# Kernel optimization log

Hardware: AMD Instinct MI355X
Metric: run time of the kernel (lower is better)

The kernel has to match this reference:

```python
import jax, jax.numpy as jnp
import numpy as np

IN_C, HID, L, NN, BS, OUT = 32, 128, 4, 64, 512, 3
N = NN * BS  # total graph vertices
EPS_LN = 1e-5
EPS_SM = 1e-16  # PyG softmax eps


def setup_inputs() -> dict:
    key = jax.random.key(0)
    ks = jax.random.split(key, 16)
    E = 524288
    x = jax.random.normal(ks[0], (N, IN_C), dtype=jnp.float32)
    edge_index = jax.random.randint(ks[1], (2, E), 0, N, dtype=jnp.int64)
    s = 0.1
    # first GAT layer (in -> hidden)
    W0 = jax.random.normal(ks[2], (IN_C, HID), dtype=jnp.float32) * s
    att_src0 = jax.random.normal(ks[3], (HID,), dtype=jnp.float32) * s
    att_dst0 = jax.random.normal(ks[4], (HID,), dtype=jnp.float32) * s
    bias0 = jnp.zeros((HID,), dtype=jnp.float32)
    # residual GAT layers (hidden -> hidden), stacked over L
    W_res = jax.random.normal(ks[5], (L, HID, HID), dtype=jnp.float32) * s
    att_src_res = jax.random.normal(ks[6], (L, HID), dtype=jnp.float32) * s
    att_dst_res = jax.random.normal(ks[7], (L, HID), dtype=jnp.float32) * s
    bias_res = jnp.zeros((L, HID), dtype=jnp.float32)
    gamma = jnp.ones((L, HID), dtype=jnp.float32)
    beta = jnp.zeros((L, HID), dtype=jnp.float32)
    # per-node predictor heads
    W1p = jax.random.normal(ks[8], (NN, HID, HID // 2), dtype=jnp.float32) * s
    W2p = jax.random.normal(ks[9], (NN, HID // 2, OUT), dtype=jnp.float32) * s
    return {"x": x, "edge_index": edge_index, "W0": W0, "att_src0": att_src0,
            "att_dst0": att_dst0, "bias0": bias0, "W_res": W_res,
            "att_src_res": att_src_res, "att_dst_res": att_dst_res,
            "bias_res": bias_res, "gamma": gamma, "beta": beta,
            "W1p": W1p, "W2p": W2p}


def _gat(x, src, dst, W, a_src, a_dst, b):
    # PyG GATConv, heads=1, negative_slope=0.2, self-loops already appended
    h = x @ W                                   # [N, H]
    a_s = (h * a_src).sum(-1)                   # [N]
    a_d = (h * a_dst).sum(-1)                   # [N]
    e = jax.nn.leaky_relu(a_s[src] + a_d[dst], 0.2)   # [E]
    m = jax.ops.segment_max(e, dst, num_segments=N)
    e = jnp.exp(e - m[dst])
    z = jax.ops.segment_sum(e, dst, num_segments=N)
    alpha = e / (z[dst] + EPS_SM)               # [E]
    out = jax.ops.segment_sum(h[src] * alpha[:, None], dst, num_segments=N)
    return out + b


def _layernorm(x, g, b):
    mu = x.mean(-1, keepdims=True)
    var = ((x - mu) ** 2).mean(-1, keepdims=True)
    return (x - mu) * jax.lax.rsqrt(var + EPS_LN) * g + b


def reference(x, edge_index, W0, att_src0, att_dst0, bias0, W_res,
              att_src_res, att_dst_res, bias_res, gamma, beta, W1p, W2p):
    loops = jnp.arange(N, dtype=edge_index.dtype)
    src = jnp.concatenate([edge_index[0], loops])
    dst = jnp.concatenate([edge_index[1], loops])
    # first GAT + relu
    h = jax.nn.relu(_gat(x, src, dst, W0, att_src0, att_dst0, bias0))
    # res+ blocks: h = h + conv(dropout(act(norm(h))))  (dropout=identity, eval)
    for i in range(L):
        t = jax.nn.relu(_layernorm(h, gamma[i], beta[i]))
        t = _gat(t, src, dst, W_res[i], att_src_res[i], att_dst_res[i], bias_res[i])
        h = h + t
    h = jax.nn.relu(_layernorm(h, gamma[0], beta[0]))
    # per-node predictor heads
    h = h.reshape(NN, BS, HID)
    t = jax.nn.relu(jnp.einsum('nbh,nhk->nbk', h, W1p))
    logits = jnp.einsum('nbk,nko->nbo', t, W2p)
    return jax.nn.softmax(logits, axis=-1)   # softmax over class dim (dim=1 per node slice)
```

## Files before the change

### kernel.cpp

```cpp
#include <hip/hip_runtime.h>
#include <hip/hip_fp8.h>
#include <math.h>

#define NND   32768
#define HIDD  128
#define NHEAD 64
#define BSS   512
#define OUTC  3
#define NTILES (NND / 16)
#define CSLOT 80

typedef _Float16 half_t;
typedef __attribute__((ext_vector_type(8))) _Float16 half8;
typedef __attribute__((ext_vector_type(4))) float f32x4;

__device__ __forceinline__ unsigned enc_fp8x4(float a, float b, float c, float d) {
    __hip_fp8x4_e4m3 q(make_float4(a, b, c, d));
    return (unsigned)q.__x;
}
__device__ __forceinline__ float4 dec_fp8x4(unsigned v) {
    __hip_fp8x4_e4m3 t; t.__x = (__hip_fp8x4_storage_t)v;
    return (float4)t;
}

__global__ __launch_bounds__(256) void prep_kernel(const float* __restrict__ W0,
        const float* __restrict__ W_res, const float* __restrict__ W1p,
        const float* __restrict__ as0, const float* __restrict__ ad0,
        const float* __restrict__ as_res, const float* __restrict__ ad_res,
        const float* __restrict__ x, const int* __restrict__ ei, int E,
        half_t* __restrict__ Wh, half_t* __restrict__ W1h, half_t* __restrict__ W0t,
        float* __restrict__ wvec, half_t* __restrict__ xh,
        int* __restrict__ counts, int* __restrict__ csrd) {
    int b = blockIdx.x, tid = threadIdx.x;
    if (b < 64) {
        __shared__ float tile[32][33];
        int l = b >> 4, t = b & 15;
        int k0 = (t >> 2) * 32, n0 = (t & 3) * 32;
        const float* src = W_res + (size_t)l * 128 * 128;
        half_t* dst = Wh + (size_t)l * 128 * 128;
        int c = tid & 31, r0 = tid >> 5;
#pragma unroll
        for (int i = 0; i < 4; ++i) tile[r0 + i * 8][c] = src[(size_t)(k0 + r0 + i * 8) * 128 + n0 + c];
        __syncthreads();
#pragma unroll
        for (int i = 0; i < 4; ++i) dst[(size_t)(n0 + r0 + i * 8) * 128 + k0 + c] = (half_t)tile[c][r0 + i * 8];
    } else if (b < 576) {
        __shared__ float tile[32][33];
        int bb = b - 64, head = bb >> 3, t = bb & 7;
        int k0 = (t >> 1) * 32, n0 = (t & 1) * 32;
        const float* src = W1p + (size_t)head * 128 * 64;
        half_t* dst = W1h + (size_t)head * 64 * 128;
        int c = tid & 31, r0 = tid >> 5;
#pragma unroll
        for (int i = 0; i < 4; ++i) tile[r0 + i * 8][c] = src[(size_t)(k0 + r0 + i * 8) * 64 + n0 + c];
        __syncthreads();
#pragma unroll
        for (int i = 0; i < 4; ++i) dst[(size_t)(n0 + r0 + i * 8) * 128 + k0 + c] = (half_t)tile[c][r0 + i * 8];
    } else if (b == 576) {
        __shared__ float t0[32][129];
        for (int i = tid; i < 4096; i += 256) t0[i >> 7][i & 127] = W0[i];
        __syncthreads();
        for (int i = tid; i < 4096; i += 256) { int n = i >> 5, k = i & 31; W0t[n * 32 + k] = (half_t)t0[k][n]; }
    } else if (b == 577) {
        for (int task = tid; task < 1088; task += 256) {
            const float* row; const float* att; int slot, sd;
            if (task < 64) {
                int k = task >> 1; sd = task & 1;
                row = W0 + k * 128; att = sd ? ad0 : as0; slot = k;
            } else {
                int tt = task - 64; int l = 1 + tt / 256; int r = tt % 256;
                int k = r >> 1; sd = r & 1;
                row = W_res + (size_t)(l - 1) * 16384 + k * 128;
                att = (sd ? ad_res : as_res) + (l - 1) * 128;
                slot = l * 128 + k;
            }
            float s = 0.f;
            for (int n = 0; n < 128; ++n) s += row[n] * att[n];
            (sd ? wvec + 640 : wvec)[slot] = s;
        }
    } else if (b < 1090) {
        int b2 = b - 578;
        const float* xs = x + (size_t)b2 * 64 * 32;
        half_t* xd = xh + (size_t)b2 * 64 * 32;
        for (int i = tid; i < 1024; i += 256) {
            float2 v = ((const float2*)xs)[i];
            union { unsigned u; half_t h[2]; } cv;
            cv.h[0] = (half_t)v.x; cv.h[1] = (half_t)v.y;
            ((unsigned*)xd)[i] = cv.u;
        }
    } else {
        int j = (b - 1090) * 256 + tid;
        int Etot = E + NND;
        if (j >= Etot) return;
        int src, dst;
        if (j < E) { src = ei[j]; dst = ei[E + j]; }
        else       { src = j - E; dst = j - E; }
        int rank = atomicAdd(&counts[dst], 1);
        if (rank < CSLOT) csrd[(size_t)dst * CSLOT + rank] = src;
    }
}

__global__ __launch_bounds__(256) void a0_kernel(const half_t* __restrict__ xh,
        const float* __restrict__ wvec,
        float* __restrict__ a_s, float* __restrict__ a_d) {
    int tid = threadIdx.x;
    __shared__ float ws0[32], wd0[32];
    if (tid < 32) { ws0[tid] = wvec[tid]; wd0[tid] = wvec[640 + tid]; }
    __syncthreads();
    int g = blockIdx.x * 256 + tid;
    int node = g >> 2, part = g & 3;
    half8 xv = *(const half8*)&xh[(size_t)node * 32 + part * 8];
    float s = 0.f, d2 = 0.f;
#pragma unroll
    for (int j = 0; j < 8; ++j) { float f = (float)xv[j]; s += f * ws0[part * 8 + j]; d2 += f * wd0[part * 8 + j]; }
    s += __shfl_xor(s, 1); s += __shfl_xor(s, 2);
    d2 += __shfl_xor(d2, 1); d2 += __shfl_xor(d2, 2);
    if (part == 0) { a_s[node] = s; a_d[node] = d2; }
}


struct MArgs {
    const half_t* xh;
    const int* csrd;
    const int* counts;
    const half_t* W0t;
    const half_t* Wh;
    const float* bias0;
    const float* b_res;
    const float* gamma;
    const float* beta;
    const float* wvec;
    float* a_s0; float* a_d0; float* a_s1; float* a_d1;
    unsigned char* Th8a; unsigned char* Th8b;
    half_t* Hh;
    const half_t* W1h;
    const float* W2p;
    float* out;
};

struct SmemT {
    half_t Pt[16][136];
    union U {
        float vv[16][132];
        struct { int s[1024]; float p[1024]; } sp;
    } u;
    int cntl[16];
    float adv[16];
};

__device__ __forceinline__ void stage_sp(const float* __restrict__ a_sv,
        const int* __restrict__ csrd, int n0, int base, int tid, SmemT& sm) {
#pragma unroll
    for (int it = 0; it < 4; ++it) {
        int i = it * 256 + tid;
        int ln = i >> 6, k = i & 63;
        int sN = 0; float pN = 0.f;
        if (base + k < sm.cntl[ln]) {
            sN = csrd[(size_t)(n0 + ln) * CSLOT + base + k];
            float tt = a_sv[sN] + sm.adv[ln];
            tt = (tt > 0.f) ? tt : 0.2f * tt;
            pN = __expf(tt);
        }
        sm.u.sp.s[i] = sN;
        sm.u.sp.p[i] = pN;
    }
}

__device__ __forceinline__ void agg2_res(const unsigned char* __restrict__ F8,
        const float* __restrict__ a_sv, const float* __restrict__ a_dv,
        const int* __restrict__ csrd, const int* __restrict__ counts,
        int n0, int tid, int wv, int lane, int q, int r15, SmemT& sm) {
    if (tid < 16) { sm.cntl[tid] = counts[n0 + tid]; sm.adv[tid] = a_dv[n0 + tid]; }
    __syncthreads();
    int maxd = 0;
    for (int i = 0; i < 16; ++i) { int d = sm.cntl[i]; maxd = d > maxd ? d : maxd; }
    float acc[4][8];
    float pz[4];
#pragma unroll
    for (int a = 0; a < 4; ++a) {
        pz[a] = 0.f;
#pragma unroll
        for (int i = 0; i < 8; ++i) acc[a][i] = 0.f;
    }
    for (int base = 0; base < maxd; base += 64) {
        __syncthreads();
        stage_sp(a_sv, csrd, n0, base, tid, sm);
        __syncthreads();
#pragma unroll
        for (int ln4 = 0; ln4 < 4; ++ln4) {
            int ln = wv * 4 + ln4;
            int rem = sm.cntl[ln] - base;
            if (rem <= 0) continue;
            int cnt = rem > 64 ? 64 : rem;
            pz[ln4] += sm.u.sp.p[ln * 64 + lane];
            const int* sl = &sm.u.sp.s[ln * 64];
            const float* pl = &sm.u.sp.p[ln * 64];
            for (int k4 = 0; k4 < cnt; k4 += 16) {
                int s0 = sl[k4 + q],      s1 = sl[k4 + 4 + q];
                int s2 = sl[k4 + 8 + q],  s3 = sl[k4 + 12 + q];
                float p0 = pl[k4 + q],    p1 = pl[k4 + 4 + q];
                float p2 = pl[k4 + 8 + q], p3 = pl[k4 + 12 + q];
                uint2 r0 = *(const uint2*)&F8[(size_t)s0 * HIDD + r15 * 8];
                uint2 r1 = *(const uint2*)&F8[(size_t)s1 * HIDD + r15 * 8];
                uint2 r2 = *(const uint2*)&F8[(size_t)s2 * HIDD + r15 * 8];
                uint2 r3 = *(const uint2*)&F8[(size_t)s3 * HIDD + r15 * 8];
                float4 f;
                f = dec_fp8x4(r0.x); acc[ln4][0]+=p0*f.x; acc[ln4][1]+=p0*f.y; acc[ln4][2]+=p0*f.z; acc[ln4][3]+=p0*f.w;
                f = dec_fp8x4(r0.y); acc[ln4][4]+=p0*f.x; acc[ln4][5]+=p0*f.y; acc[ln4][6]+=p0*f.z; acc[ln4][7]+=p0*f.w;
                f = dec_fp8x4(r1.x); acc[ln4][0]+=p1*f.x; acc[ln4][1]+=p1*f.y; acc[ln4][2]+=p1*f.z; acc[ln4][3]+=p1*f.w;
                f = dec_fp8x4(r1.y); acc[ln4][4]+=p1*f.x; acc[ln4][5]+=p1*f.y; acc[ln4][6]+=p1*f.z; acc[ln4][7]+=p1*f.w;
                f = dec_fp8x4(r2.x); acc[ln4][0]+=p2*f.x; acc[ln4][1]+=p2*f.y; acc[ln4][2]+=p2*f.z; acc[ln4][3]+=p2*f.w;
                f = dec_fp8x4(r2.y); acc[ln4][4]+=p2*f.x; acc[ln4][5]+=p2*f.y; acc[ln4][6]+=p2*f.z; acc[ln4][7]+=p2*f.w;
                f = dec_fp8x4(r3.x); acc[ln4][0]+=p3*f.x; acc[ln4][1]+=p3*f.y; acc[ln4][2]+=p3*f.z; acc[ln4][3]+=p3*f.w;
                f = dec_fp8x4(r3.y); acc[ln4][4]+=p3*f.x; acc[ln4][5]+=p3*f.y; acc[ln4][6]+=p3*f.z; acc[ln4][7]+=p3*f.w;
            }
        }
    }
#pragma unroll
    for (int ln4 = 0; ln4 < 4; ++ln4) {
        int ln = wv * 4 + ln4;
        float z = pz[ln4];
#pragma unroll
        for (int o = 32; o; o >>= 1) z += __shfl_xor(z, o);
#pragma unroll
        for (int i = 0; i < 8; ++i) {
            acc[ln4][i] += __shfl_xor(acc[ln4][i], 16);
            acc[ln4][i] += __shfl_xor(acc[ln4][i], 32);
        }
        if (q == 0) {
            float inv = 1.f / (z + 1e-16f);
            union { int4 v; half_t hh[8]; } u;
#pragma unroll
            for (int i = 0; i < 8; ++i) u.hh[i] = (half_t)(acc[ln4][i] * inv);
            *(int4*)&sm.Pt[ln][r15 * 8] = u.v;
        }
    }
}

__device__ __forceinline__ void agg2_l0(const half_t* __restrict__ xh,
        const float* __restrict__ a_sv, const float* __restrict__ a_dv,
        const int* __restrict__ csrd, const int* __restrict__ counts,
        int n0, int tid, int wv, int lane, int q, int r15, SmemT& sm) {
    if (tid < 16) { sm.cntl[tid] = counts[n0 + tid]; sm.adv[tid] = a_dv[n0 + tid]; }
    __syncthreads();
    int maxd = 0;
    for (int i = 0; i < 16; ++i) { int d = sm.cntl[i]; maxd = d > maxd ? d : maxd; }
    float acc[4][2];
    float pz[4];
#pragma unroll
    for (int a = 0; a < 4; ++a) { pz[a] = 0.f; acc[a][0] = 0.f; acc[a][1] = 0.f; }
    for (int base = 0; base < maxd; base += 64) {
        __syncthreads();
        stage_sp(a_sv, csrd, n0, base, tid, sm);
        __syncthreads();
#pragma unroll
        for (int ln4 = 0; ln4 < 4; ++ln4) {
            int ln = wv * 4 + ln4;
            int rem = sm.cntl[ln] - base;
            if (rem <= 0) continue;
            int cnt = rem > 64 ? 64 : rem;
            pz[ln4] += sm.u.sp.p[ln * 64 + lane];
            const int* sl = &sm.u.sp.s[ln * 64];
            const float* pl = &sm.u.sp.p[ln * 64];
            for (int k4 = 0; k4 < cnt; k4 += 16) {
                int s0 = sl[k4 + q],      s1 = sl[k4 + 4 + q];
                int s2 = sl[k4 + 8 + q],  s3 = sl[k4 + 12 + q];
                float p0 = pl[k4 + q],    p1 = pl[k4 + 4 + q];
                float p2 = pl[k4 + 8 + q], p3 = pl[k4 + 12 + q];
                union { unsigned u; half_t h[2]; } u0, u1, u2, u3;
                u0.u = *(const unsigned*)&xh[(size_t)s0 * 32 + r15 * 2];
                u1.u = *(const unsigned*)&xh[(size_t)s1 * 32 + r15 * 2];
                u2.u = *(const unsigned*)&xh[(size_t)s2 * 32 + r15 * 2];
                u3.u = *(const unsigned*)&xh[(size_t)s3 * 32 + r15 * 2];
                acc[ln4][0] += p0 * (float)u0.h[0] + p1 * (float)u1.h[0] + p2 * (float)u2.h[0] + p3 * (float)u3.h[0];
                acc[ln4][1] += p0 * (float)u0.h[1] + p1 * (float)u1.h[1] + p2 * (float)u2.h[1] + p3 * (float)u3.h[1];
            }
        }
    }
#pragma unroll
    for (int ln4 = 0; ln4 < 4; ++ln4) {
        int ln = wv * 4 + ln4;
        float z = pz[ln4];
#pragma unroll
        for (int o = 32; o; o >>= 1) z += __shfl_xor(z, o);
#pragma unroll
        for (int i = 0; i < 2; ++i) {
            acc[ln4][i] += __shfl_xor(acc[ln4][i], 16);
            acc[ln4][i] += __shfl_xor(acc[ln4][i], 32);
        }
        if (q == 0) {
            float inv = 1.f / (z + 1e-16f);
            union { unsigned u; half_t h[2]; } w2;
            w2.h[0] = (half_t)(acc[ln4][0] * inv);
            w2.h[1] = (half_t)(acc[ln4][1] * inv);
            *(unsigned*)&sm.Pt[ln][r15 * 2] = w2.u;
        }
    }
}

template <int K, bool RES>
__device__ __forceinline__ void gemm_epi_tile(int n0, int tid, int wv, int q, int r15,
        const half_t* __restrict__ Whl, const float* __restrict__ bias,
        half_t* __restrict__ Hh, unsigned char* __restrict__ Th8o,
        const float* __restrict__ gamma, const float* __restrict__ beta,
        const float* __restrict__ wsn, const float* __restrict__ wdn,
        float* __restrict__ as_out, float* __restrict__ ad_out,
        half_t Pt[16][136], float vv[16][132]) {
    half8 afrag[K / 32];
#pragma unroll
    for (int s = 0; s < K / 32; ++s)
        afrag[s] = *(const half8*)&Pt[r15][s * 32 + q * 8];
    f32x4 acc2[2];
#pragma unroll
    for (int i = 0; i < 2; ++i) {
        int ct = wv * 2 + i;
        f32x4 c = {0.f, 0.f, 0.f, 0.f};
#pragma unroll
        for (int s = 0; s < K / 32; ++s) {
            half8 bfrag = *(const half8*)&Whl[(size_t)(ct * 16 + r15) * K + s * 32 + q * 8];
            c = __builtin_amdgcn_mfma_f32_16x16x32_f16(afrag[s], bfrag, c, 0, 0, 0);
        }
        acc2[i] = c;
    }
#pragma unroll
    for (int i = 0; i < 2; ++i)
#pragma unroll
        for (int r = 0; r < 4; ++r)
            vv[q * 4 + r][wv * 32 + i * 16 + r15] = acc2[i][r];
    __syncthreads();
    int grp = tid >> 4, sub = tid & 15;
    float4 bi0 = *(const float4*)&bias[sub * 8],  bi1 = *(const float4*)&bias[sub * 8 + 4];
    float4 g0  = *(const float4*)&gamma[sub * 8], g1  = *(const float4*)&gamma[sub * 8 + 4];
    float4 be0 = *(const float4*)&beta[sub * 8],  be1 = *(const float4*)&beta[sub * 8 + 4];
    float4 ws0 = *(const float4*)&wsn[sub * 8],   ws1 = *(const float4*)&wsn[sub * 8 + 4];
    float4 wd0 = *(const float4*)&wdn[sub * 8],   wd1 = *(const float4*)&wdn[sub * 8 + 4];
    float bi[8] = {bi0.x,bi0.y,bi0.z,bi0.w,bi1.x,bi1.y,bi1.z,bi1.w};
    float gg[8] = {g0.x,g0.y,g0.z,g0.w,g1.x,g1.y,g1.z,g1.w};
    float be[8] = {be0.x,be0.y,be0.z,be0.w,be1.x,be1.y,be1.z,be1.w};
    float ws[8] = {ws0.x,ws0.y,ws0.z,ws0.w,ws1.x,ws1.y,ws1.z,ws1.w};
    float wd[8] = {wd0.x,wd0.y,wd0.z,wd0.w,wd1.x,wd1.y,wd1.z,wd1.w};
    int node = n0 + grp;
    float v8[8];
#pragma unroll
    for (int j = 0; j < 8; ++j) v8[j] = vv[grp][sub * 8 + j] + bi[j];
    if (RES) {
        half8 hold = *(const half8*)&Hh[(size_t)node * HIDD + sub * 8];
#pragma unroll
        for (int j = 0; j < 8; ++j) v8[j] += (float)hold[j];
    } else {
#pragma unroll
        for (int j = 0; j < 8; ++j) v8[j] = fmaxf(v8[j], 0.f);
    }
    union { int4 i4; half_t h[8]; } hw;
#pragma unroll
    for (int j = 0; j < 8; ++j) hw.h[j] = (half_t)v8[j];
    *(int4*)&Hh[(size_t)node * HIDD + sub * 8] = hw.i4;
    float sum = 0.f;
#pragma unroll
    for (int j = 0; j < 8; ++j) sum += v8[j];
#pragma unroll
    for (int o = 8; o; o >>= 1) sum += __shfl_xor(sum, o);
    float mu = sum * (1.f / HIDD);
    float var = 0.f;
#pragma unroll
    for (int j = 0; j < 8; ++j) { float dx = v8[j] - mu; var += dx * dx; }
#pragma unroll
    for (int o = 8; o; o >>= 1) var += __shfl_xor(var, o);
    float rs = rsqrtf(var * (1.f / HIDD) + 1e-5f);
    float tt[8];
    float asn = 0.f, adn = 0.f;
#pragma unroll
    for (int j = 0; j < 8; ++j) {
        float t = fmaxf((v8[j] - mu) * rs * gg[j] + be[j], 0.f);
        tt[j] = t;
        asn += t * ws[j];
        adn += t * wd[j];
    }
    uint2 tw;
    tw.x = enc_fp8x4(tt[0], tt[1], tt[2], tt[3]);
    tw.y = enc_fp8x4(tt[4], tt[5], tt[6], tt[7]);
    *(uint2*)&Th8o[(size_t)node * HIDD + sub * 8] = tw;
#pragma unroll
    for (int o = 8; o; o >>= 1) { asn += __shfl_xor(asn, o); adn += __shfl_xor(adn, o); }
    if (sub == 0) { as_out[node] = asn; ad_out[node] = adn; }
}

__device__ __forceinline__ void last_tile(int n0, int tid, int wv, int q, int r15,
        const MArgs& A, half_t Pt[16][136], float vv[16][132]) {
    const half_t* Whl = A.Wh + (size_t)3 * 16384;
    half8 afrag[4];
#pragma unroll
    for (int s = 0; s < 4; ++s)
        afrag[s] = *(const half8*)&Pt[r15][s * 32 + q * 8];
    f32x4 acc2[2];
#pragma unroll
    for (int i = 0; i < 2; ++i) {
        int ct = wv * 2 + i;
        f32x4 c = {0.f, 0.f, 0.f, 0.f};
#pragma unroll
        for (int s = 0; s < 4; ++s) {
            half8 bfrag = *(const half8*)&Whl[(size_t)(ct * 16 + r15) * 128 + s * 32 + q * 8];
            c = __builtin_amdgcn_mfma_f32_16x16x32_f16(afrag[s], bfrag, c, 0, 0, 0);
        }
        acc2[i] = c;
    }
#pragma unroll
    for (int i = 0; i < 2; ++i)
#pragma unroll
        for (int r = 0; r < 4; ++r)
            vv[q * 4 + r][wv * 32 + i * 16 + r15] = acc2[i][r];
    __syncthreads();
    int grp = tid >> 4, sub = tid & 15;
    const float* bias = A.b_res + 3 * HIDD;
    float4 bi0 = *(const float4*)&bias[sub * 8],    bi1 = *(const float4*)&bias[sub * 8 + 4];
    float4 g0  = *(const float4*)&A.gamma[sub * 8], g1  = *(const float4*)&A.gamma[sub * 8 + 4];
    float4 be0 = *(const float4*)&A.beta[sub * 8],  be1 = *(const float4*)&A.beta[sub * 8 + 4];
    float bi[8] = {bi0.x,bi0.y,bi0.z,bi0.w,bi1.x,bi1.y,bi1.z,bi1.w};
    float gg[8] = {g0.x,g0.y,g0.z,g0.w,g1.x,g1.y,g1.z,g1.w};
    float be[8] = {be0.x,be0.y,be0.z,be0.w,be1.x,be1.y,be1.z,be1.w};
    int node = n0 + grp;
    float v8[8];
    half8 hold = *(const half8*)&A.Hh[(size_t)node * HIDD + sub * 8];
#pragma unroll
    for (int j = 0; j < 8; ++j) v8[j] = vv[grp][sub * 8 + j] + bi[j] + (float)hold[j];
    float sum = 0.f;
#pragma unroll
    for (int j = 0; j < 8; ++j) sum += v8[j];
#pragma unroll
    for (int o = 8; o; o >>= 1) sum += __shfl_xor(sum, o);
    float mu = sum * (1.f / HIDD);
    float var = 0.f;
#pragma unroll
    for (int j = 0; j < 8; ++j) { float dx = v8[j] - mu; var += dx * dx; }
#pragma unroll
    for (int o = 8; o; o >>= 1) var += __shfl_xor(var, o);
    float rs = rsqrtf(var * (1.f / HIDD) + 1e-5f);
    union { int4 i4; half_t h[8]; } u;
#pragma unroll
    for (int j = 0; j < 8; ++j)
        u.h[j] = (half_t)fmaxf((v8[j] - mu) * rs * gg[j] + be[j], 0.f);
    __syncthreads();
    *(int4*)&Pt[grp][sub * 8] = u.i4;
    __syncthreads();
    int head = n0 >> 9;
    const half_t* W1g = A.W1h + (size_t)head * 64 * 128;
    half8 pa[4];
#pragma unroll
    for (int s = 0; s < 4; ++s)
        pa[s] = *(const half8*)&Pt[r15][s * 32 + q * 8];
    int n2 = wv * 16 + r15;
    f32x4 c = {0.f, 0.f, 0.f, 0.f};
#pragma unroll
    for (int s = 0; s < 4; ++s) {
        half8 bfrag = *(const half8*)&W1g[(size_t)n2 * 128 + s * 32 + q * 8];
        c = __builtin_amdgcn_mfma_f32_16x16x32_f16(pa[s], bfrag, c, 0, 0, 0);
    }
    float w2a = A.W2p[(size_t)head * 192 + n2 * 3 + 0];
    float w2b = A.W2p[(size_t)head * 192 + n2 * 3 + 1];
    float w2c = A.W2p[(size_t)head * 192 + n2 * 3 + 2];
    float lg[3][4];
#pragma unroll
    for (int r = 0; r < 4; ++r) {
        float t = fmaxf(c[r], 0.f);
        lg[0][r] = t * w2a;
        lg[1][r] = t * w2b;
        lg[2][r] = t * w2c;
    }
#pragma unroll
    for (int o = 8; o; o >>= 1)
#pragma unroll
        for (int oo = 0; oo < 3; ++oo)
#pragma unroll
            for (int r = 0; r < 4; ++r) lg[oo][r] += __shfl_xor(lg[oo][r], o);
    __syncthreads();
    if (r15 == 0) {
#pragma unroll
        for (int r = 0; r < 4; ++r)
#pragma unroll
            for (int oo = 0; oo < 3; ++oo) vv[q * 4 + r][wv * 3 + oo] = lg[oo][r];
    }
    __syncthreads();
    if (tid < 16) {
        float l0 = vv[tid][0] + vv[tid][3] + vv[tid][6] + vv[tid][9];
        float l1 = vv[tid][1] + vv[tid][4] + vv[tid][7] + vv[tid][10];
        float l2 = vv[tid][2] + vv[tid][5] + vv[tid][8] + vv[tid][11];
        float mx = fmaxf(l0, fmaxf(l1, l2));
        float e0 = __expf(l0 - mx), e1 = __expf(l1 - mx), e2 = __expf(l2 - mx);
        float inv = 1.f / (e0 + e1 + e2);
        float* op = A.out + (size_t)(n0 + tid) * OUTC;
        op[0] = e0 * inv; op[1] = e1 * inv; op[2] = e2 * inv;
    }
}

__global__ __launch_bounds__(256, 4) void fused3_l0(MArgs A) {
    __shared__ SmemT sm;
    int tid = threadIdx.x;
    int wv = tid >> 6, lane = tid & 63;
    int q = lane >> 4, r15 = lane & 15;
    int n0 = blockIdx.x * 16;
    agg2_l0(A.xh, A.a_s0, A.a_d0, A.csrd, A.counts, n0, tid, wv, lane, q, r15, sm);
    __syncthreads();
    gemm_epi_tile<32, false>(n0, tid, wv, q, r15, A.W0t, A.bias0, A.Hh, A.Th8a,
        A.gamma, A.beta, A.wvec + 128, A.wvec + 640 + 128, A.a_s1, A.a_d1, sm.Pt, sm.u.vv);
}

template <int L>
__global__ __launch_bounds__(256, 4) void fused3_res(MArgs A) {
    __shared__ SmemT sm;
    int tid = threadIdx.x;
    int wv = tid >> 6, lane = tid & 63;
    int q = lane >> 4, r15 = lane & 15;
    int n0 = blockIdx.x * 16;
    const unsigned char* Ts = (L & 1) ? A.Th8b : A.Th8a;
    unsigned char* Td       = (L & 1) ? A.Th8a : A.Th8b;
    const float* asv = (L & 1) ? A.a_s0 : A.a_s1;
    const float* adv = (L & 1) ? A.a_d0 : A.a_d1;
    float* aso = (L & 1) ? A.a_s1 : A.a_s0;
    float* ado = (L & 1) ? A.a_d1 : A.a_d0;
    agg2_res(Ts, asv, adv, A.csrd, A.counts, n0, tid, wv, lane, q, r15, sm);
    __syncthreads();
    gemm_epi_tile<128, true>(n0, tid, wv, q, r15, A.Wh + (size_t)L * 16384,
        A.b_res + L * HIDD, A.Hh, Td, A.gamma + (L + 1) * HIDD, A.beta + (L + 1) * HIDD,
        A.wvec + (L + 2) * 128, A.wvec + 640 + (L + 2) * 128, aso, ado, sm.Pt, sm.u.vv);
}

__global__ __launch_bounds__(256, 4) void fused3_last(MArgs A) {
    __shared__ SmemT sm;
    int tid = threadIdx.x;
    int wv = tid >> 6, lane = tid & 63;
    int q = lane >> 4, r15 = lane & 15;
    int n0 = blockIdx.x * 16;
    agg2_res(A.Th8b, A.a_s0, A.a_d0, A.csrd, A.counts, n0, tid, wv, lane, q, r15, sm);
    __syncthreads();
    last_tile(n0, tid, wv, q, r15, A, sm.Pt, sm.u.vv);
}

extern "C" void kernel_launch(void* const* d_in, const int* in_sizes, int n_in,
                              void* d_out, int out_size, void* d_ws, size_t ws_size,
                              hipStream_t stream) {
    const float* x        = (const float*)d_in[0];
    const int*   ei       = (const int*)d_in[1];
    const float* W0       = (const float*)d_in[2];
    const float* att_src0 = (const float*)d_in[3];
    const float* att_dst0 = (const float*)d_in[4];
    const float* bias0    = (const float*)d_in[5];
    const float* W_res    = (const float*)d_in[6];
    const float* as_res   = (const float*)d_in[7];
    const float* ad_res   = (const float*)d_in[8];
    const float* b_res    = (const float*)d_in[9];
    const float* gamma    = (const float*)d_in[10];
    const float* beta     = (const float*)d_in[11];
    const float* W1p      = (const float*)d_in[12];
    const float* W2p      = (const float*)d_in[13];
    float* out = (float*)d_out;

    int E = in_sizes[1] / 2;
    int Etot = E + NND;

    char* p = (char*)d_ws;
    auto alloc = [&](size_t bytes) { void* r = (void*)p; p += (bytes + 255) & ~(size_t)255; return r; };
    int*    counts  = (int*)alloc((size_t)NND * 4);
    int*    csrd    = (int*)alloc((size_t)NND * CSLOT * 4);
    half_t* xh      = (half_t*)alloc((size_t)NND * 32 * 2);
    unsigned char* Th8a = (unsigned char*)alloc((size_t)NND * HIDD);
    unsigned char* Th8b = (unsigned char*)alloc((size_t)NND * HIDD);
    half_t* Hh      = (half_t*)alloc((size_t)NND * HIDD * 2);
    float*  a_s0    = (float*)alloc((size_t)NND * 4);
    float*  a_d0    = (float*)alloc((size_t)NND * 4);
    float*  a_s1    = (float*)alloc((size_t)NND * 4);
    float*  a_d1    = (float*)alloc((size_t)NND * 4);
    half_t* Wh      = (half_t*)alloc((size_t)4 * HIDD * HIDD * 2);
    half_t* W1h     = (half_t*)alloc((size_t)NHEAD * 64 * HIDD * 2);
    half_t* W0t     = (half_t*)alloc((size_t)HIDD * 32 * 2);
    float*  wvec    = (float*)alloc((size_t)1280 * 4);

    int egrid = (Etot + 255) / 256;

    hipMemsetAsync(counts, 0, (size_t)NND * 4, stream);
    prep_kernel<<<1090 + egrid, 256, 0, stream>>>(W0, W_res, W1p, att_src0, att_dst0,
        as_res, ad_res, x, ei, E, Wh, W1h, W0t, wvec, xh, counts, csrd);
    a0_kernel<<<512, 256, 0, stream>>>(xh, wvec, a_s0, a_d0);

    MArgs ma;
    ma.xh = xh; ma.csrd = csrd; ma.counts = counts;
    ma.W0t = W0t; ma.Wh = Wh;
    ma.bias0 = bias0; ma.b_res = b_res;
    ma.gamma = gamma; ma.beta = beta; ma.wvec = wvec;
    ma.a_s0 = a_s0; ma.a_d0 = a_d0; ma.a_s1 = a_s1; ma.a_d1 = a_d1;
    ma.Th8a = Th8a; ma.Th8b = Th8b; ma.Hh = Hh;
    ma.W1h = W1h; ma.W2p = W2p; ma.out = out;

    fused3_l0<<<NTILES, 256, 0, stream>>>(ma);
    fused3_res<0><<<NTILES, 256, 0, stream>>>(ma);
    fused3_res<1><<<NTILES, 256, 0, stream>>>(ma);
    fused3_res<2><<<NTILES, 256, 0, stream>>>(ma);
    fused3_last<<<NTILES, 256, 0, stream>>>(ma);
}
```

Measured before the change: 277.6 us.

## Cut register pressure in GAT aggregation and epilogue to raise occupancy

Splits the residual aggregation into two passes of two nodes each, so only 2x8 accumulators are live instead of 4x8. Adds a fast path that stages neighbor data once when every node in the tile has at most 64 edges. Reorders the epilogue to load gamma, beta and the attention vectors in smaller chunks, and raises launch bounds to 8 waves per SIMD for the l0 and residual kernels. The goal is higher occupancy to hide gather latency. In exchange, the multi-chunk path now restages the CSR slice once per pass, and the tighter register cap risks spills.

```diff
diff --git a/kernel.cpp b/kernel.cpp
--- a/kernel.cpp
+++ b/kernel.cpp
@@ -31,9 +31,9 @@
         half_t* __restrict__ Wh, half_t* __restrict__ W1h, half_t* __restrict__ W0t,
         float* __restrict__ wvec, half_t* __restrict__ xh,
         int* __restrict__ counts, int* __restrict__ csrd) {
+    __shared__ float tile[32][129];
     int b = blockIdx.x, tid = threadIdx.x;
     if (b < 64) {
-        __shared__ float tile[32][33];
         int l = b >> 4, t = b & 15;
         int k0 = (t >> 2) * 32, n0 = (t & 3) * 32;
         const float* src = W_res + (size_t)l * 128 * 128;
@@ -45,7 +45,6 @@
 #pragma unroll
         for (int i = 0; i < 4; ++i) dst[(size_t)(n0 + r0 + i * 8) * 128 + k0 + c] = (half_t)tile[c][r0 + i * 8];
     } else if (b < 576) {
-        __shared__ float tile[32][33];
         int bb = b - 64, head = bb >> 3, t = bb & 7;
         int k0 = (t >> 1) * 32, n0 = (t & 1) * 32;
         const float* src = W1p + (size_t)head * 128 * 64;
@@ -57,10 +56,9 @@
 #pragma unroll
         for (int i = 0; i < 4; ++i) dst[(size_t)(n0 + r0 + i * 8) * 128 + k0 + c] = (half_t)tile[c][r0 + i * 8];
     } else if (b == 576) {
-        __shared__ float t0[32][129];
-        for (int i = tid; i < 4096; i += 256) t0[i >> 7][i & 127] = W0[i];
+        for (int i = tid; i < 4096; i += 256) tile[i >> 7][i & 127] = W0[i];
         __syncthreads();
-        for (int i = tid; i < 4096; i += 256) { int n = i >> 5, k = i & 31; W0t[n * 32 + k] = (half_t)t0[k][n]; }
+        for (int i = tid; i < 4096; i += 256) { int n = i >> 5, k = i & 31; W0t[n * 32 + k] = (half_t)tile[k][n]; }
     } else if (b == 577) {
         for (int task = tid; task < 1088; task += 256) {
             const float* row; const float* att; int slot, sd;
@@ -166,6 +164,59 @@
     }
 }
 
+__device__ __forceinline__ void agg_node_f8(const unsigned char* __restrict__ F8,
+        const SmemT& sm, int ln, int base, int lane, int q, int r15,
+        float acc[8], float& pzv) {
+    int rem = sm.cntl[ln] - base;
+    if (rem <= 0) return;
+    int cnt = rem > 64 ? 64 : rem;
+    pzv += sm.u.sp.p[ln * 64 + lane];
+    const int* sl = &sm.u.sp.s[ln * 64];
+    const float* pl = &sm.u.sp.p[ln * 64];
+    for (int k4 = 0; k4 < cnt; k4 += 16) {
+        int s0 = sl[k4 + q],       s1 = sl[k4 + 4 + q];
+        int s2 = sl[k4 + 8 + q],   s3 = sl[k4 + 12 + q];
+        float p0 = pl[k4 + q],     p1 = pl[k4 + 4 + q];
+        float p2 = pl[k4 + 8 + q], p3 = pl[k4 + 12 + q];
+        uint2 r0 = *(const uint2*)&F8[(size_t)s0 * HIDD + r15 * 8];
+        uint2 r1 = *(const uint2*)&F8[(size_t)s1 * HIDD + r15 * 8];
+        uint2 r2 = *(const uint2*)&F8[(size_t)s2 * HIDD + r15 * 8];
+        uint2 r3 = *(const uint2*)&F8[(size_t)s3 * HIDD + r15 * 8];
+        float4 f;
+        f = dec_fp8x4(r0.x); acc[0]+=p0*f.x; acc[1]+=p0*f.y; acc[2]+=p0*f.z; acc[3]+=p0*f.w;
+        f = dec_fp8x4(r0.y); acc[4]+=p0*f.x; acc[5]+=p0*f.y; acc[6]+=p0*f.z; acc[7]+=p0*f.w;
+        f = dec_fp8x4(r1.x); acc[0]+=p1*f.x; acc[1]+=p1*f.y; acc[2]+=p1*f.z; acc[3]+=p1*f.w;
+        f = dec_fp8x4(r1.y); acc[4]+=p1*f.x; acc[5]+=p1*f.y; acc[6]+=p1*f.z; acc[7]+=p1*f.w;
+        f = dec_fp8x4(r2.x); acc[0]+=p2*f.x; acc[1]+=p2*f.y; acc[2]+=p2*f.z; acc[3]+=p2*f.w;
+        f = dec_fp8x4(r2.y); acc[4]+=p2*f.x; acc[5]+=p2*f.y; acc[6]+=p2*f.z; acc[7]+=p2*f.w;
+        f = dec_fp8x4(r3.x); acc[0]+=p3*f.x; acc[1]+=p3*f.y; acc[2]+=p3*f.z; acc[3]+=p3*f.w;
+        f = dec_fp8x4(r3.y); acc[4]+=p3*f.x; acc[5]+=p3*f.y; acc[6]+=p3*f.z; acc[7]+=p3*f.w;
+    }
+}
+
+__device__ __forceinline__ void finish_res(SmemT& sm, int wv, int pass, int q, int r15,
+        float acc[2][8], float pz2[2]) {
+#pragma unroll
+    for (int ln2 = 0; ln2 < 2; ++ln2) {
+        int ln = wv * 4 + pass * 2 + ln2;
+        float z = pz2[ln2];
+#pragma unroll
+        for (int o = 32; o; o >>= 1) z += __shfl_xor(z, o);
+#pragma unroll
+        for (int i = 0; i < 8; ++i) {
+            acc[ln2][i] += __shfl_xor(acc[ln2][i], 16);
+            acc[ln2][i] += __shfl_xor(acc[ln2][i], 32);
+        }
+        if (q == 0) {
+            float inv = 1.f / (z + 1e-16f);
+            union { int4 v; half_t hh[8]; } u;
+#pragma unroll
+            for (int i = 0; i < 8; ++i) u.hh[i] = (half_t)(acc[ln2][i] * inv);
+            *(int4*)&sm.Pt[ln][r15 * 8] = u.v;
+        }
+    }
+}
+
 __device__ __forceinline__ void agg2_res(const unsigned char* __restrict__ F8,
         const float* __restrict__ a_sv, const float* __restrict__ a_dv,
         const int* __restrict__ csrd, const int* __restrict__ counts,
@@ -174,65 +225,40 @@
     __syncthreads();
     int maxd = 0;
     for (int i = 0; i < 16; ++i) { int d = sm.cntl[i]; maxd = d > maxd ? d : maxd; }
-    float acc[4][8];
-    float pz[4];
-#pragma unroll
-    for (int a = 0; a < 4; ++a) {
-        pz[a] = 0.f;
-#pragma unroll
-        for (int i = 0; i < 8; ++i) acc[a][i] = 0.f;
-    }
-    for (int base = 0; base < maxd; base += 64) {
+    if (maxd <= 64) {
+        stage_sp(a_sv, csrd, n0, 0, tid, sm);
         __syncthreads();
-        stage_sp(a_sv, csrd, n0, base, tid, sm);
-        __syncthreads();
-#pragma unroll
-        for (int ln4 = 0; ln4 < 4; ++ln4) {
-            int ln = wv * 4 + ln4;
-            int rem = sm.cntl[ln] - base;
-            if (rem <= 0) continue;
-            int cnt = rem > 64 ? 64 : rem;
-            pz[ln4] += sm.u.sp.p[ln * 64 + lane];
-            const int* sl = &sm.u.sp.s[ln * 64];
-            const float* pl = &sm.u.sp.p[ln * 64];
-            for (int k4 = 0; k4 < cnt; k4 += 16) {
-                int s0 = sl[k4 + q],      s1 = sl[k4 + 4 + q];
-                int s2 = sl[k4 + 8 + q],  s3 = sl[k4 + 12 + q];
-                float p0 = pl[k4 + q],    p1 = pl[k4 + 4 + q];
-                float p2 = pl[k4 + 8 + q], p3 = pl[k4 + 12 + q];
-                uint2 r0 = *(const uint2*)&F8[(size_t)s0 * HIDD + r15 * 8];
-                uint2 r1 = *(const uint2*)&F8[(size_t)s1 * HIDD + r15 * 8];
-                uint2 r2 = *(const uint2*)&F8[(size_t)s2 * HIDD + r15 * 8];
-                uint2 r3 = *(const uint2*)&F8[(size_t)s3 * HIDD + r15 * 8];
-                float4 f;
-                f = dec_fp8x4(r0.x); acc[ln4][0]+=p0*f.x; acc[ln4][1]+=p0*f.y; acc[ln4][2]+=p0*f.z; acc[ln4][3]+=p0*f.w;
-                f = dec_fp8x4(r0.y); acc[ln4][4]+=p0*f.x; acc[ln4][5]+=p0*f.y; acc[ln4][6]+=p0*f.z; acc[ln4][7]+=p0*f.w;
-                f = dec_fp8x4(r1.x); acc[ln4][0]+=p1*f.x; acc[ln4][1]+=p1*f.y; acc[ln4][2]+=p1*f.z; acc[ln4][3]+=p1*f.w;
-                f = dec_fp8x4(r1.y); acc[ln4][4]+=p1*f.x; acc[ln4][5]+=p1*f.y; acc[ln4][6]+=p1*f.z; acc[ln4][7]+=p1*f.w;
-                f = dec_fp8x4(r2.x); acc[ln4][0]+=p2*f.x; acc[ln4][1]+=p2*f.y; acc[ln4][2]+=p2*f.z; acc[ln4][3]+=p2*f.w;
-                f = dec_fp8x4(r2.y); acc[ln4][4]+=p2*f.x; acc[ln4][5]+=p2*f.y; acc[ln4][6]+=p2*f.z; acc[ln4][7]+=p2*f.w;
-                f = dec_fp8x4(r3.x); acc[ln4][0]+=p3*f.x; acc[ln4][1]+=p3*f.y; acc[ln4][2]+=p3*f.z; acc[ln4][3]+=p3*f.w;
-                f = dec_fp8x4(r3.y); acc[ln4][4]+=p3*f.x; acc[ln4][5]+=p3*f.y; acc[ln4][6]+=p3*f.z; acc[ln4][7]+=p3*f.w;
+#pragma unroll
+        for (int pass = 0; pass < 2; ++pass) {
+            float acc[2][8];
+            float pz2[2] = {0.f, 0.f};
+#pragma unroll
+            for (int a = 0; a < 2; ++a)
+#pragma unroll
+                for (int i = 0; i < 8; ++i) acc[a][i] = 0.f;
+#pragma unroll
+            for (int ln2 = 0; ln2 < 2; ++ln2)
+                agg_node_f8(F8, sm, wv * 4 + pass * 2 + ln2, 0, lane, q, r15, acc[ln2], pz2[ln2]);
+            finish_res(sm, wv, pass, q, r15, acc, pz2);
+        }
+    } else {
+#pragma unroll
+        for (int pass = 0; pass < 2; ++pass) {
+            float acc[2][8];
+            float pz2[2] = {0.f, 0.f};
+#pragma unroll
+            for (int a = 0; a < 2; ++a)
+#pragma unroll
+                for (int i = 0; i < 8; ++i) acc[a][i] = 0.f;
+            for (int base = 0; base < maxd; base += 64) {
+                __syncthreads();
+                stage_sp(a_sv, csrd, n0, base, tid, sm);
+                __syncthreads();
+#pragma unroll
+                for (int ln2 = 0; ln2 < 2; ++ln2)
+                    agg_node_f8(F8, sm, wv * 4 + pass * 2 + ln2, base, lane, q, r15, acc[ln2], pz2[ln2]);
             }
-        }
-    }
-#pragma unroll
-    for (int ln4 = 0; ln4 < 4; ++ln4) {
-        int ln = wv * 4 + ln4;
-        float z = pz[ln4];
-#pragma unroll
-        for (int o = 32; o; o >>= 1) z += __shfl_xor(z, o);
-#pragma unroll
-        for (int i = 0; i < 8; ++i) {
-            acc[ln4][i] += __shfl_xor(acc[ln4][i], 16);
-            acc[ln4][i] += __shfl_xor(acc[ln4][i], 32);
-        }
-        if (q == 0) {
-            float inv = 1.f / (z + 1e-16f);
-            union { int4 v; half_t hh[8]; } u;
-#pragma unroll
-            for (int i = 0; i < 8; ++i) u.hh[i] = (half_t)(acc[ln4][i] * inv);
-            *(int4*)&sm.Pt[ln][r15 * 8] = u.v;
+            finish_res(sm, wv, pass, q, r15, acc, pz2);
         }
     }
 }
@@ -329,20 +355,17 @@
             vv[q * 4 + r][wv * 32 + i * 16 + r15] = acc2[i][r];
     __syncthreads();
     int grp = tid >> 4, sub = tid & 15;
-    float4 bi0 = *(const float4*)&bias[sub * 8],  bi1 = *(const float4*)&bias[sub * 8 + 4];
-    float4 g0  = *(const float4*)&gamma[sub * 8], g1  = *(const float4*)&gamma[sub * 8 + 4];
-    float4 be0 = *(const float4*)&beta[sub * 8],  be1 = *(const float4*)&beta[sub * 8 + 4];
-    float4 ws0 = *(const float4*)&wsn[sub * 8],   ws1 = *(const float4*)&wsn[sub * 8 + 4];
-    float4 wd0 = *(const float4*)&wdn[sub * 8],   wd1 = *(const float4*)&wdn[sub * 8 + 4];
-    float bi[8] = {bi0.x,bi0.y,bi0.z,bi0.w,bi1.x,bi1.y,bi1.z,bi1.w};
-    float gg[8] = {g0.x,g0.y,g0.z,g0.w,g1.x,g1.y,g1.z,g1.w};
-    float be[8] = {be0.x,be0.y,be0.z,be0.w,be1.x,be1.y,be1.z,be1.w};
-    float ws[8] = {ws0.x,ws0.y,ws0.z,ws0.w,ws1.x,ws1.y,ws1.z,ws1.w};
-    float wd[8] = {wd0.x,wd0.y,wd0.z,wd0.w,wd1.x,wd1.y,wd1.z,wd1.w};
     int node = n0 + grp;
+    const float* vrow = &vv[grp][sub * 8];
     float v8[8];
-#pragma unroll
-    for (int j = 0; j < 8; ++j) v8[j] = vv[grp][sub * 8 + j] + bi[j];
+    {
+        float4 bi0 = *(const float4*)&bias[sub * 8];
+        float4 bi1 = *(const float4*)&bias[sub * 8 + 4];
+        v8[0] = vrow[0] + bi0.x; v8[1] = vrow[1] + bi0.y;
+        v8[2] = vrow[2] + bi0.z; v8[3] = vrow[3] + bi0.w;
+        v8[4] = vrow[4] + bi1.x; v8[5] = vrow[5] + bi1.y;
+        v8[6] = vrow[6] + bi1.z; v8[7] = vrow[7] + bi1.w;
+    }
     if (RES) {
         half8 hold = *(const half8*)&Hh[(size_t)node * HIDD + sub * 8];
 #pragma unroll
@@ -367,18 +390,34 @@
 #pragma unroll
     for (int o = 8; o; o >>= 1) var += __shfl_xor(var, o);
     float rs = rsqrtf(var * (1.f / HIDD) + 1e-5f);
-    float tt[8];
-    float asn = 0.f, adn = 0.f;
-#pragma unroll
-    for (int j = 0; j < 8; ++j) {
-        float t = fmaxf((v8[j] - mu) * rs * gg[j] + be[j], 0.f);
-        tt[j] = t;
-        asn += t * ws[j];
-        adn += t * wd[j];
-    }
+    float asn, adn;
     uint2 tw;
-    tw.x = enc_fp8x4(tt[0], tt[1], tt[2], tt[3]);
-    tw.y = enc_fp8x4(tt[4], tt[5], tt[6], tt[7]);
+    {
+        float4 g4 = *(const float4*)&gamma[sub * 8];
+        float4 b4 = *(const float4*)&beta[sub * 8];
+        float t0 = fmaxf((v8[0] - mu) * rs * g4.x + b4.x, 0.f);
+        float t1 = fmaxf((v8[1] - mu) * rs * g4.y + b4.y, 0.f);
+        float t2 = fmaxf((v8[2] - mu) * rs * g4.z + b4.z, 0.f);
+        float t3 = fmaxf((v8[3] - mu) * rs * g4.w + b4.w, 0.f);
+        float4 w4 = *(const float4*)&wsn[sub * 8];
+        float4 d4 = *(const float4*)&wdn[sub * 8];
+        asn = t0 * w4.x; asn += t1 * w4.y; asn += t2 * w4.z; asn += t3 * w4.w;
+        adn = t0 * d4.x; adn += t1 * d4.y; adn += t2 * d4.z; adn += t3 * d4.w;
+        tw.x = enc_fp8x4(t0, t1, t2, t3);
+    }
+    {
+        float4 g4 = *(const float4*)&gamma[sub * 8 + 4];
+        float4 b4 = *(const float4*)&beta[sub * 8 + 4];
+        float t4 = fmaxf((v8[4] - mu) * rs * g4.x + b4.x, 0.f);
+        float t5 = fmaxf((v8[5] - mu) * rs * g4.y + b4.y, 0.f);
+        float t6 = fmaxf((v8[6] - mu) * rs * g4.z + b4.z, 0.f);
+        float t7 = fmaxf((v8[7] - mu) * rs * g4.w + b4.w, 0.f);
+        float4 w4 = *(const float4*)&wsn[sub * 8 + 4];
+        float4 d4 = *(const float4*)&wdn[sub * 8 + 4];
+        asn += t4 * w4.x; asn += t5 * w4.y; asn += t6 * w4.z; asn += t7 * w4.w;
+        adn += t4 * d4.x; adn += t5 * d4.y; adn += t6 * d4.z; adn += t7 * d4.w;
+        tw.y = enc_fp8x4(t4, t5, t6, t7);
+    }
     *(uint2*)&Th8o[(size_t)node * HIDD + sub * 8] = tw;
 #pragma unroll
     for (int o = 8; o; o >>= 1) { asn += __shfl_xor(asn, o); adn += __shfl_xor(adn, o); }
@@ -492,7 +531,7 @@
     }
 }
 
-__global__ __launch_bounds__(256, 4) void fused3_l0(MArgs A) {
+__global__ __launch_bounds__(256, 8) void fused6_l0(MArgs A) {
     __shared__ SmemT sm;
     int tid = threadIdx.x;
     int wv = tid >> 6, lane = tid & 63;
@@ -505,7 +544,7 @@
 }
 
 template <int L>
-__global__ __launch_bounds__(256, 4) void fused3_res(MArgs A) {
+__global__ __launch_bounds__(256, 8) void fused6_res(MArgs A) {
     __shared__ SmemT sm;
     int tid = threadIdx.x;
     int wv = tid >> 6, lane = tid & 63;
@@ -524,7 +563,7 @@
         A.wvec + (L + 2) * 128, A.wvec + 640 + (L + 2) * 128, aso, ado, sm.Pt, sm.u.vv);
 }
 
-__global__ __launch_bounds__(256, 4) void fused3_last(MArgs A) {
+__global__ __launch_bounds__(256, 4) void fused6_last(MArgs A) {
     __shared__ SmemT sm;
     int tid = threadIdx.x;
     int wv = tid >> 6, lane = tid & 63;
@@ -590,9 +629,9 @@
     ma.Th8a = Th8a; ma.Th8b = Th8b; ma.Hh = Hh;
     ma.W1h = W1h; ma.W2p = W2p; ma.out = out;
 
-    fused3_l0<<<NTILES, 256, 0, stream>>>(ma);
-    fused3_res<0><<<NTILES, 256, 0, stream>>>(ma);
-    fused3_res<1><<<NTILES, 256, 0, stream>>>(ma);
-    fused3_res<2><<<NTILES, 256, 0, stream>>>(ma);
-    fused3_last<<<NTILES, 256, 0, stream>>>(ma);
-}
+    fused6_l0<<<NTILES, 256, 0, stream>>>(ma);
+    fused6_res<0><<<NTILES, 256, 0, stream>>>(ma);
+    fused6_res<1><<<NTILES, 256, 0, stream>>>(ma);
+    fused6_res<2><<<NTILES, 256, 0, stream>>>(ma);
+    fused6_last<<<NTILES, 256, 0, stream>>>(ma);
+}
```

Result: slower. 292.7 us (+5.4%).
